# Kernel optimization log

Hardware: AMD Instinct MI355X
Metric: run time of the kernel (lower is better)

Reference implementation:

```python
import jax, jax.numpy as jnp
import numpy as np

NUM_HEADS = 4
KERNEL = 7
DILATION = 1
EMBED = 128
CTX = 256
RANK = 8
HEAD_DIM = EMBED // NUM_HEADS
SCALE = HEAD_DIM ** (-0.5)


def setup_inputs() -> dict:
    key = jax.random.key(0)
    ks = jax.random.split(key, 16)
    B, H, W = 4, 64, 64
    inp = {
        "x": jax.random.normal(ks[0], (B, H, W, EMBED), jnp.float32),
        "context": jax.random.normal(ks[1], (B, CTX), jnp.float32),
        # base QKV linear (torch Linear: y = x @ W.T + b)
        "Wqkv": jax.random.normal(ks[2], (3 * EMBED, EMBED), jnp.float32) * 0.02,
        "bqkv": jax.random.normal(ks[3], (3 * EMBED,), jnp.float32) * 0.02,
        # bilinear LoRA params (init scale 0.01 as in source)
        "A": jax.random.normal(ks[4], (EMBED, RANK), jnp.float32) * 0.01,
        "Blora": jax.random.normal(ks[5], (CTX, RANK), jnp.float32) * 0.01,
        "Vlora": jax.random.normal(ks[6], (3 * EMBED, RANK), jnp.float32) * 0.01,
        # gate MLP: Linear(ctx,16) -> ReLU -> Linear(16,1) -> Sigmoid
        "g1w": jax.random.normal(ks[7], (16, CTX), jnp.float32) * 0.05,
        "g1b": jnp.zeros((16,), jnp.float32),
        "g2w": jnp.full((1, 16), -5.0, jnp.float32) * 0.0 + jax.random.normal(ks[8], (1, 16), jnp.float32) * 0.01 - 5.0 / 16.0,
        "g2b": jnp.full((1,), -5.0, jnp.float32),
        # output projection
        "Wproj": jax.random.normal(ks[9], (EMBED, EMBED), jnp.float32) * 0.02,
        "bproj": jnp.zeros((EMBED,), jnp.float32),
    }
    return inp


def _windows(t, H, W):
    # t: [B, nh, H+2p, W+2p, d] -> [B, nh, H, W, K^2, d]
    ws = []
    for i in range(KERNEL):
        for j in range(KERNEL):
            ws.append(t[:, :, i * DILATION:i * DILATION + H, j * DILATION:j * DILATION + W, :])
    return jnp.stack(ws, axis=4)


def reference(x, context, Wqkv, bqkv, A, Blora, Vlora, g1w, g1b, g2w, g2b, Wproj, bproj):
    B, H, W, C = x.shape
    nh, hd = NUM_HEADS, HEAD_DIM
    # context-modulated QKV: base + alpha * ((xA) * (cB)) V^T
    base = x @ Wqkv.T + bqkv                                   # [B,H,W,3C]
    c_proj = context @ Blora                                   # [B,r]
    delta = ((x @ A) * c_proj[:, None, None, :]) @ Vlora.T     # [B,H,W,3C]
    alpha = jax.nn.sigmoid(jax.nn.relu(context @ g1w.T + g1b) @ g2w.T + g2b)  # [B,1]
    qkv = base + alpha[:, None, None, :] * delta               # [B,H,W,3C]

    qkv = qkv.reshape(B, H, W, 3, nh, hd)
    qkv = jnp.transpose(qkv, (3, 0, 4, 1, 2, 5))               # [3,B,nh,H,W,hd]
    q, k, v = qkv[0], qkv[1], qkv[2]

    pad = DILATION * (KERNEL - 1) // 2
    pw = ((0, 0), (0, 0), (pad, pad), (pad, pad), (0, 0))
    k_p = jnp.pad(k, pw)
    v_p = jnp.pad(v, pw)
    kw = _windows(k_p, H, W)                                   # [B,nh,H,W,K2,hd]
    vw = _windows(v_p, H, W)

    attn = jnp.einsum('bnijd,bnijkd->bnijk', q, kw) * SCALE    # [B,nh,H,W,K2]
    attn = jax.nn.softmax(attn, axis=-1)
    out = jnp.einsum('bnijk,bnijkd->bnijd', attn, vw)          # [B,nh,H,W,hd]

    out = jnp.transpose(out, (0, 2, 3, 1, 4)).reshape(B, H, W, C)
    out = out @ Wproj.T + bproj
    return out
```

## Files before the change

### kernel.cpp

```cpp
#include <hip/hip_runtime.h>
#include <cstddef>

#define CTXDIM 256
#define RANK 8
#define SCALE 0.17677669529663687f
#define WSTRIDE 136

#define WF0 0
#define QS0 8704
#define KL0 17408
#define VT0 53248
#define SMSZ 77824
#define KHEAD 8960
#define VHEAD 8192

typedef _Float16 half8 __attribute__((ext_vector_type(8)));
typedef _Float16 half2_t __attribute__((ext_vector_type(2)));
typedef float floatx4 __attribute__((ext_vector_type(4)));
typedef float floatx16 __attribute__((ext_vector_type(16)));
typedef int intx4 __attribute__((ext_vector_type(4)));

struct Params {
  const float *x, *ctx, *Wqkv, *bqkv, *A, *Blora, *Vlora;
  const float *g1w, *g1b, *g2w, *g2b, *Wproj, *bproj;
  float* out;
};

__device__ __forceinline__ void stage_rows_f16_512(const float* __restrict__ src,
                                                   _Float16* dst, int tid) {
  const int row = tid >> 2;
  const int c0 = (tid & 3) * 32;
  const float* sp = src + (size_t)row * 128 + c0;
  _Float16* dp = dst + row * WSTRIDE + c0;
#pragma unroll
  for (int i = 0; i < 4; ++i) {
    const float4 a = *(const float4*)(sp + i * 8);
    const float4 b = *(const float4*)(sp + i * 8 + 4);
    half8 o;
    o[0] = (_Float16)a.x; o[1] = (_Float16)a.y;
    o[2] = (_Float16)a.z; o[3] = (_Float16)a.w;
    o[4] = (_Float16)b.x; o[5] = (_Float16)b.y;
    o[6] = (_Float16)b.z; o[7] = (_Float16)b.w;
    *(half8*)(dp + i * 8) = o;
  }
}

__device__ __forceinline__ int vta(int d, int k) {
  const int sig = (d + (d >> 3)) & 7;
  return d * 256 + (((k >> 3) ^ sig) << 3) + (k & 7);
}

__device__ __forceinline__ int packh(float x, float y) {
  half2_t h;
  h[0] = (_Float16)x;
  h[1] = (_Float16)y;
  return __builtin_bit_cast(int, h);
}

template <int MT0>
__device__ __forceinline__ floatx16 attn_wave(const _Float16* kls,
                                              const _Float16* vtl,
                                              half8 qb0, half8 qb1,
                                              int m31, int l5, int pi, int pj) {
  const floatx16 zz = {0.f,0.f,0.f,0.f,0.f,0.f,0.f,0.f,
                       0.f,0.f,0.f,0.f,0.f,0.f,0.f,0.f};
  floatx16 acc[5];
#pragma unroll
  for (int mt = 0; mt < 5; ++mt) {
    const int Mt = MT0 + mt;
    const half8 ka0 = *(const half8*)&kls[(Mt * 32 + m31) * 40 + l5 * 8];
    const half8 ka1 = *(const half8*)&kls[(Mt * 32 + m31) * 40 + 16 + l5 * 8];
    floatx16 a = zz;
    a = __builtin_amdgcn_mfma_f32_32x32x16_f16(ka0, qb0, a, 0, 0, 0);
    a = __builtin_amdgcn_mfma_f32_32x32x16_f16(ka1, qb1, a, 0, 0, 0);
    acc[mt] = a;
  }

  bool vR[14];
#pragma unroll
  for (int i = 0; i < 14; ++i) vR[i] = (unsigned)(i - pi) < 7u;
  bool vC[8];
#pragma unroll
  for (int c8 = 0; c8 < 8; ++c8) {
    const int hcv = (c8 & 3) + 8 * (c8 >> 2) + 4 * l5;
    vC[c8] = (unsigned)(hcv - pj) < 7u;
  }

  float mxp[4] = {-1e30f, -1e30f, -1e30f, -1e30f};
#pragma unroll
  for (int mt = 0; mt < 5; ++mt) {
#pragma unroll
    for (int reg = 0; reg < 16; ++reg) {
      const bool v = vR[2 * (MT0 + mt) + (reg >> 3)] &&
                     vC[(reg & 3) + 4 * ((reg >> 2) & 1)];
      const float x = v ? acc[mt][reg] : -1e30f;
      acc[mt][reg] = x;
      mxp[reg & 3] = fmaxf(mxp[reg & 3], x);
    }
  }
  float mx = fmaxf(fmaxf(mxp[0], mxp[1]), fmaxf(mxp[2], mxp[3]));
  mx = fmaxf(mx, __shfl_xor(mx, 32, 64));

  const float SC2 = SCALE * 1.4426950408889634f;
  float sp[4] = {0.f, 0.f, 0.f, 0.f};
#pragma unroll
  for (int mt = 0; mt < 5; ++mt) {
#pragma unroll
    for (int reg = 0; reg < 16; ++reg) {
      const float pv = exp2f((acc[mt][reg] - mx) * SC2);
      acc[mt][reg] = pv;
      sp[reg & 3] += pv;
    }
  }
  float sum = (sp[0] + sp[1]) + (sp[2] + sp[3]);
  sum += __shfl_xor(sum, 32, 64);
  const float inv = 1.f / sum;

  floatx16 oacc = zz;
  const int sigd = (m31 + (m31 >> 3)) & 7;
  const int vbase = m31 * 256;
#pragma unroll
  for (int kk = 0; kk < 10; ++kk) {
    const int ks = MT0 * 2 + kk;
    const int mt = (ks >> 1) - MT0;
    const int r8 = 8 * (ks & 1);
    const int E00 = packh(acc[mt][r8 + 0] * inv, acc[mt][r8 + 1] * inv);
    const int E01 = packh(acc[mt][r8 + 2] * inv, acc[mt][r8 + 3] * inv);
    const int E10 = packh(acc[mt][r8 + 4] * inv, acc[mt][r8 + 5] * inv);
    const int E11 = packh(acc[mt][r8 + 6] * inv, acc[mt][r8 + 7] * inv);
    const int R00 = __shfl_xor(E00, 32, 64);
    const int R01 = __shfl_xor(E01, 32, 64);
    const int R10 = __shfl_xor(E10, 32, 64);
    const int R11 = __shfl_xor(E11, 32, 64);
    const int A0 = l5 ? R10 : E00;
    const int A1 = l5 ? R11 : E01;
    const int A2 = l5 ? E10 : R00;
    const int A3 = l5 ? E11 : R01;
    const intx4 ai = {A0, A1, A2, A3};
    const half8 af = __builtin_bit_cast(half8, ai);
    const half8 vb = *(const half8*)&vtl[vbase + (((2 * ks + l5) ^ sigd) << 3)];
    oacc = __builtin_amdgcn_mfma_f32_32x32x16_f16(af, vb, oacc, 0, 0, 0);
  }
  return oacc;
}

__global__ __launch_bounds__(512, 1) void mono_kernel(Params p) {
  __shared__ __align__(16) _Float16 sm[SMSZ];
  __shared__ float cal_s[8];

  const int bid = blockIdx.x;
  const int tj = bid & 7;
  const int ti = (bid >> 3) & 7;
  const int b  = bid >> 6;
  const int tid = threadIdx.x;
  const int lane = tid & 63;
  const int w = tid >> 6;
  const int m31 = lane & 31;
  const int l5 = lane >> 5;
  const int i0 = ti * 8 - 3;
  const int j0 = tj * 8 - 3;

  _Float16* wfold = sm + WF0;
  _Float16* qs    = sm + QS0;
  _Float16* kls   = sm + KL0;
  _Float16* vtl   = sm + VT0;

  const floatx16 zz = {0.f,0.f,0.f,0.f,0.f,0.f,0.f,0.f,
                       0.f,0.f,0.f,0.f,0.f,0.f,0.f,0.f};
  const int sigd = (m31 + (m31 >> 3)) & 7;

  auto load_xrow = [&](int rowlin, half8* xr) {
#pragma unroll
    for (int ks = 0; ks < 8; ++ks) xr[ks] = (half8){0, 0, 0, 0, 0, 0, 0, 0};
    if (rowlin < 196) {
      const int hr = rowlin / 14;
      const int hc = rowlin - hr * 14;
      const int ii = i0 + hr;
      const int jj = j0 + hc;
      if ((unsigned)ii < 64u && (unsigned)jj < 64u) {
        const float* xp = p.x + (size_t)(b * 4096 + ii * 64 + jj) * 128 + l5 * 8;
#pragma unroll
        for (int ks = 0; ks < 8; ++ks) {
          const float4 a = *(const float4*)(xp + ks * 16);
          const float4 c = *(const float4*)(xp + ks * 16 + 4);
          half8 o;
          o[0] = (_Float16)a.x; o[1] = (_Float16)a.y;
          o[2] = (_Float16)a.z; o[3] = (_Float16)a.w;
          o[4] = (_Float16)c.x; o[5] = (_Float16)c.y;
          o[6] = (_Float16)c.z; o[7] = (_Float16)c.w;
          xr[ks] = o;
        }
      }
    }
  };

  const int mtq = (w & 3) + 1;
  const int chq = w >> 2;
  half8 xrq[8];
  load_xrow(mtq * 32 + m31, xrq);

  if (w == 0) {
    const float c0 = p.ctx[b * CTXDIM + lane];
    const float c1 = p.ctx[b * CTXDIM + 64 + lane];
    const float c2 = p.ctx[b * CTXDIM + 128 + lane];
    const float c3 = p.ctx[b * CTXDIM + 192 + lane];
    float cp[RANK];
#pragma unroll
    for (int r = 0; r < RANK; ++r) {
      float q = c0 * p.Blora[lane * RANK + r] + c1 * p.Blora[(64 + lane) * RANK + r] +
                c2 * p.Blora[(128 + lane) * RANK + r] + c3 * p.Blora[(192 + lane) * RANK + r];
#pragma unroll
      for (int s = 32; s; s >>= 1) q += __shfl_xor(q, s, 64);
      cp[r] = q;
    }
    float gacc = 0.f;
#pragma unroll
    for (int h = 0; h < 16; ++h) {
      float q = c0 * p.g1w[h * CTXDIM + lane] + c1 * p.g1w[h * CTXDIM + 64 + lane] +
                c2 * p.g1w[h * CTXDIM + 128 + lane] + c3 * p.g1w[h * CTXDIM + 192 + lane];
#pragma unroll
      for (int s = 32; s; s >>= 1) q += __shfl_xor(q, s, 64);
      gacc += fmaxf(q + p.g1b[h], 0.f) * p.g2w[h];
    }
    if (lane == 0) {
      const float alpha = 1.f / (1.f + __expf(-(gacc + p.g2b[0])));
#pragma unroll
      for (int r = 0; r < RANK; ++r) cal_s[r] = alpha * cp[r];
    }
  }

  for (int idx = tid; idx < 2688; idx += 512) {
    const int hd = idx / 896;
    const int r2 = idx - hd * 896;
    const int d = r2 & 31;
    const int kk = r2 >> 5;
    const int k = (kk >> 1) * 16 + 14 + (kk & 1);
    vtl[hd * VHEAD + vta(d, k)] = (_Float16)0.f;
  }

  const int kq = tid & 127;
  const int hgrp = tid >> 7;
  const float4 a0 = *(const float4*)&p.A[kq * RANK];
  const float4 a1 = *(const float4*)&p.A[kq * RANK + 4];

  __syncthreads();

  const float* cb = cal_s;
  const float t0 = a0.x * cb[0], t1 = a0.y * cb[1];
  const float t2 = a0.z * cb[2], t3 = a0.w * cb[3];
  const float t4 = a1.x * cb[4], t5 = a1.y * cb[5];
  const float t6 = a1.z * cb[6], t7 = a1.w * cb[7];

  auto FOLD = [&](int n0) {
#pragma unroll
    for (int rr = 0; rr < 16; ++rr) {
      const int row = hgrp * 16 + rr;
      const int o = n0 + row;
      const float4 v0 = *(const float4*)&p.Vlora[o * RANK];
      const float4 v1 = *(const float4*)&p.Vlora[o * RANK + 4];
      float d = t0 * v0.x;
      d = fmaf(t1, v0.y, d);
      d = fmaf(t2, v0.z, d);
      d = fmaf(t3, v0.w, d);
      d = fmaf(t4, v1.x, d);
      d = fmaf(t5, v1.y, d);
      d = fmaf(t6, v1.z, d);
      d = fmaf(t7, v1.w, d);
      wfold[row * WSTRIDE + kq] = (_Float16)(p.Wqkv[o * 128 + kq] + d);
    }
  };

  auto QGEMM = [&](int i) {
    const int n0 = i * 64;
    const int nc = n0 + chq * 32 + m31;
    const float bq = p.bqkv[nc];
    floatx16 c = zz;
    const _Float16* br = &wfold[(chq * 32 + m31) * WSTRIDE + l5 * 8];
#pragma unroll
    for (int ks = 0; ks < 8; ++ks) {
      const half8 f = *(const half8*)(br + ks * 16);
      c = __builtin_amdgcn_mfma_f32_32x32x16_f16(xrq[ks], f, c, 0, 0, 0);
    }
#pragma unroll
    for (int reg = 0; reg < 16; ++reg) {
      const int rowlin = mtq * 32 + (reg & 3) + 8 * (reg >> 2) + 4 * l5;
      const int hr = rowlin / 14;
      const int hc = rowlin - hr * 14;
      if ((unsigned)(hr - 3) < 8u && (unsigned)(hc - 3) < 8u) {
        const int px = (hr - 3) * 8 + (hc - 3);
        qs[px * 136 + nc] = (_Float16)(c[reg] + bq);
      }
    }
  };

  FOLD(0);   __syncthreads(); QGEMM(0); __syncthreads();
  FOLD(64);  __syncthreads(); QGEMM(1); __syncthreads();

  half8 xrkv[8];
  load_xrow(w * 32 + m31, xrkv);
  floatx16 v3save = zz;

  auto KVGEMM = [&](int it) {
    const int n0 = it * 64;
    const float bh0 = p.bqkv[n0 + m31];
    const float bh1 = p.bqkv[n0 + 32 + m31];
    if (w < 7) {
      floatx16 c0 = zz, c1 = zz;
      const _Float16* b0r = &wfold[m31 * WSTRIDE + l5 * 8];
      const _Float16* b1r = &wfold[(32 + m31) * WSTRIDE + l5 * 8];
#pragma unroll
      for (int ks = 0; ks < 8; ++ks) {
        const half8 f0 = *(const half8*)(b0r + ks * 16);
        const half8 f1 = *(const half8*)(b1r + ks * 16);
        c0 = __builtin_amdgcn_mfma_f32_32x32x16_f16(xrkv[ks], f0, c0, 0, 0, 0);
        c1 = __builtin_amdgcn_mfma_f32_32x32x16_f16(xrkv[ks], f1, c1, 0, 0, 0);
      }
#pragma unroll
      for (int reg = 0; reg < 16; ++reg) {
        const int rowlin = w * 32 + (reg & 3) + 8 * (reg >> 2) + 4 * l5;
        if (rowlin < 196) {
          const int hr = rowlin / 14;
          const int hc = rowlin - hr * 14;
          const int hp = hr * 16 + hc;
          const bool ok = (unsigned)(i0 + hr) < 64u && (unsigned)(j0 + hc) < 64u;
          const float v0 = ok ? c0[reg] + bh0 : 0.f;
          const float v1 = ok ? c1[reg] + bh1 : 0.f;
          const int off = (((hp >> 3) ^ sigd) << 3) | (hp & 7);
          if (it == 2) {
            kls[hp * 40 + m31] = (_Float16)v0;
            kls[KHEAD + hp * 40 + m31] = (_Float16)v1;
          } else if (it == 3) {
            kls[2 * KHEAD + hp * 40 + m31] = (_Float16)v0;
            kls[3 * KHEAD + hp * 40 + m31] = (_Float16)v1;
          } else if (it == 4) {
            vtl[m31 * 256 + off] = (_Float16)v0;
            vtl[VHEAD + m31 * 256 + off] = (_Float16)v1;
          } else {
            vtl[2 * VHEAD + m31 * 256 + off] = (_Float16)v0;
            v3save[reg] = v1;
          }
        }
      }
    }
  };

  FOLD(128); __syncthreads(); KVGEMM(2); __syncthreads();
  FOLD(192); __syncthreads(); KVGEMM(3); __syncthreads();
  FOLD(256); __syncthreads(); KVGEMM(4); __syncthreads();
  FOLD(320); __syncthreads(); KVGEMM(5); __syncthreads();

  for (int idx = tid; idx < 896; idx += 512) {
    const int d = idx & 31;
    const int kk = idx >> 5;
    const int k = (kk >> 1) * 16 + 14 + (kk & 1);
    wfold[vta(d, k)] = (_Float16)0.f;
  }
  if (w < 7) {
#pragma unroll
    for (int reg = 0; reg < 16; ++reg) {
      const int rowlin = w * 32 + (reg & 3) + 8 * (reg >> 2) + 4 * l5;
      if (rowlin < 196) {
        const int hr = rowlin / 14;
        const int hc = rowlin - hr * 14;
        const int hp = hr * 16 + hc;
        const int off = (((hp >> 3) ^ sigd) << 3) | (hp & 7);
        wfold[m31 * 256 + off] = (_Float16)v3save[reg];
      }
    }
  }
  __syncthreads();

  const int hh = w >> 1;
  const int half_ = w & 1;
  const int pixA = half_ * 32 + m31;
  const int piA = pixA >> 3, pjA = pixA & 7;
  const half8 qb0 = *(const half8*)&qs[pixA * 136 + hh * 32 + l5 * 8];
  const half8 qb1 = *(const half8*)&qs[pixA * 136 + hh * 32 + 16 + l5 * 8];
  const _Float16* kpp = kls + hh * KHEAD;
  const _Float16* vpp = (hh < 3) ? (vtl + hh * VHEAD) : wfold;

  const floatx16 oA = half_ ? attn_wave<2>(kpp, vpp, qb0, qb1, m31, l5, piA, pjA)
                            : attn_wave<0>(kpp, vpp, qb0, qb1, m31, l5, piA, pjA);
  __syncthreads();

  _Float16* at_s = kls;
  _Float16* wsh  = kls + 64 * WSTRIDE;
#pragma unroll
  for (int reg = 0; reg < 16; ++reg) {
    const int rowM = (reg & 3) + 8 * (reg >> 2) + 4 * l5;
    at_s[(half_ * 32 + rowM) * WSTRIDE + hh * 32 + m31] = (_Float16)oA[reg];
  }
  stage_rows_f16_512(p.Wproj, wsh, tid);
  __syncthreads();

  const int r = lane & 15;
  const int quad = lane >> 4;
  const int rw = w & 3;
  const int nh = w >> 2;
  const _Float16* ap = at_s + (rw * 16 + r) * WSTRIDE + quad * 8;
  const _Float16* bp = wsh + (nh * 64 + r) * WSTRIDE + quad * 8;
  floatx4 acc[4];
#pragma unroll
  for (int nt = 0; nt < 4; ++nt) acc[nt] = (floatx4){0.f, 0.f, 0.f, 0.f};
#pragma unroll
  for (int kc = 0; kc < 4; ++kc) {
    const half8 a = *(const half8*)(ap + kc * 32);
#pragma unroll
    for (int nt = 0; nt < 4; ++nt) {
      const half8 bf = *(const half8*)(bp + nt * 16 * WSTRIDE + kc * 32);
      acc[nt] = __builtin_amdgcn_mfma_f32_16x16x32_f16(a, bf, acc[nt], 0, 0, 0);
    }
  }

  const int rbase = b * 4096 + (ti * 8 + rw * 2 + (quad >> 1)) * 64 +
                    tj * 8 + (quad & 1) * 4;
  float bv[4];
#pragma unroll
  for (int nt = 0; nt < 4; ++nt) bv[nt] = p.bproj[nh * 64 + nt * 16 + r];
#pragma unroll
  for (int reg = 0; reg < 4; ++reg) {
    float* cp = p.out + (size_t)(rbase + reg) * 128 + nh * 64;
#pragma unroll
    for (int nt = 0; nt < 4; ++nt)
      cp[nt * 16 + r] = acc[nt][reg] + bv[nt];
  }
}

extern "C" void kernel_launch(void* const* d_in, const int* in_sizes, int n_in,
                              void* d_out, int out_size, void* d_ws, size_t ws_size,
                              hipStream_t stream) {
  Params hp;
  hp.x     = (const float*)d_in[0];
  hp.ctx   = (const float*)d_in[1];
  hp.Wqkv  = (const float*)d_in[2];
  hp.bqkv  = (const float*)d_in[3];
  hp.A     = (const float*)d_in[4];
  hp.Blora = (const float*)d_in[5];
  hp.Vlora = (const float*)d_in[6];
  hp.g1w   = (const float*)d_in[7];
  hp.g1b   = (const float*)d_in[8];
  hp.g2w   = (const float*)d_in[9];
  hp.g2b   = (const float*)d_in[10];
  hp.Wproj = (const float*)d_in[11];
  hp.bproj = (const float*)d_in[12];
  hp.out   = (float*)d_out;

  mono_kernel<<<256, 512, 0, stream>>>(hp);
}
```

Before: 46.80 us.

## Switch neighborhood attention softmax to online per-tile form with deferred normalization

The per-wave attention now fuses QK scores, masking, exponentiation and the PV MFMA tile by tile, using an online-softmax running max and sum. Rescaling is skipped unless the tile max exceeds the running max by a threshold, and the 1/sum normalization moves to the epilogue store. This removes the five live 32x32 score accumulators, cutting register pressure and the separate max/exp/sum passes. It adds wave-wide votes and shuffles, and launch bounds now request two blocks per CU, which caps registers but may not fit the large LDS footprint.

```diff
diff --git a/kernel.cpp b/kernel.cpp
--- a/kernel.cpp
+++ b/kernel.cpp
@@ -61,10 +61,27 @@
 __device__ __forceinline__ floatx16 attn_wave(const _Float16* kls,
                                               const _Float16* vtl,
                                               half8 qb0, half8 qb1,
-                                              int m31, int l5, int pi, int pj) {
+                                              int m31, int l5, int pi, int pj,
+                                              float& inv_out) {
   const floatx16 zz = {0.f,0.f,0.f,0.f,0.f,0.f,0.f,0.f,
                        0.f,0.f,0.f,0.f,0.f,0.f,0.f,0.f};
-  floatx16 acc[5];
+  bool vR[14];
+#pragma unroll
+  for (int i = 0; i < 14; ++i) vR[i] = (unsigned)(i - pi) < 7u;
+  bool vC[8];
+#pragma unroll
+  for (int c8 = 0; c8 < 8; ++c8) {
+    const int hcv = (c8 & 3) + 8 * (c8 >> 2) + 4 * l5;
+    vC[c8] = (unsigned)(hcv - pj) < 7u;
+  }
+
+  const float SC2 = SCALE * 1.4426950408889634f;
+  const int sigd = (m31 + (m31 >> 3)) & 7;
+  const int vbase = m31 * 256;
+
+  floatx16 oacc = zz;
+  float m = -1e30f, s = 0.f;
+
 #pragma unroll
   for (int mt = 0; mt < 5; ++mt) {
     const int Mt = MT0 + mt;
@@ -73,78 +90,66 @@
     floatx16 a = zz;
     a = __builtin_amdgcn_mfma_f32_32x32x16_f16(ka0, qb0, a, 0, 0, 0);
     a = __builtin_amdgcn_mfma_f32_32x32x16_f16(ka1, qb1, a, 0, 0, 0);
-    acc[mt] = a;
-  }
-
-  bool vR[14];
-#pragma unroll
-  for (int i = 0; i < 14; ++i) vR[i] = (unsigned)(i - pi) < 7u;
-  bool vC[8];
-#pragma unroll
-  for (int c8 = 0; c8 < 8; ++c8) {
-    const int hcv = (c8 & 3) + 8 * (c8 >> 2) + 4 * l5;
-    vC[c8] = (unsigned)(hcv - pj) < 7u;
-  }
-
-  float mxp[4] = {-1e30f, -1e30f, -1e30f, -1e30f};
-#pragma unroll
-  for (int mt = 0; mt < 5; ++mt) {
+
+    float pmax = -1e30f;
 #pragma unroll
     for (int reg = 0; reg < 16; ++reg) {
-      const bool v = vR[2 * (MT0 + mt) + (reg >> 3)] &&
+      const bool v = vR[2 * Mt + (reg >> 3)] &&
                      vC[(reg & 3) + 4 * ((reg >> 2) & 1)];
-      const float x = v ? acc[mt][reg] : -1e30f;
-      acc[mt][reg] = x;
-      mxp[reg & 3] = fmaxf(mxp[reg & 3], x);
-    }
-  }
-  float mx = fmaxf(fmaxf(mxp[0], mxp[1]), fmaxf(mxp[2], mxp[3]));
-  mx = fmaxf(mx, __shfl_xor(mx, 32, 64));
-
-  const float SC2 = SCALE * 1.4426950408889634f;
-  float sp[4] = {0.f, 0.f, 0.f, 0.f};
-#pragma unroll
-  for (int mt = 0; mt < 5; ++mt) {
+      const float x = v ? a[reg] : -1e30f;
+      a[reg] = x;
+      pmax = fmaxf(pmax, x);
+    }
+    const float pmaxp = fmaxf(pmax, __shfl_xor(pmax, 32, 64));
+
+    if (!__all(pmaxp - m <= 16.f)) {
+      const float mnew = fmaxf(m, pmaxp);
+      const float f = exp2f((m - mnew) * SC2);
+      s *= f;
+#pragma unroll
+      for (int reg = 0; reg < 16; ++reg) {
+        const int rowM = (reg & 3) + 8 * (reg >> 2) + 4 * l5;
+        oacc[reg] *= __shfl(f, rowM, 64);
+      }
+      m = mnew;
+    }
+
 #pragma unroll
     for (int reg = 0; reg < 16; ++reg) {
-      const float pv = exp2f((acc[mt][reg] - mx) * SC2);
-      acc[mt][reg] = pv;
-      sp[reg & 3] += pv;
-    }
-  }
-  float sum = (sp[0] + sp[1]) + (sp[2] + sp[3]);
-  sum += __shfl_xor(sum, 32, 64);
-  const float inv = 1.f / sum;
-
-  floatx16 oacc = zz;
-  const int sigd = (m31 + (m31 >> 3)) & 7;
-  const int vbase = m31 * 256;
-#pragma unroll
-  for (int kk = 0; kk < 10; ++kk) {
-    const int ks = MT0 * 2 + kk;
-    const int mt = (ks >> 1) - MT0;
-    const int r8 = 8 * (ks & 1);
-    const int E00 = packh(acc[mt][r8 + 0] * inv, acc[mt][r8 + 1] * inv);
-    const int E01 = packh(acc[mt][r8 + 2] * inv, acc[mt][r8 + 3] * inv);
-    const int E10 = packh(acc[mt][r8 + 4] * inv, acc[mt][r8 + 5] * inv);
-    const int E11 = packh(acc[mt][r8 + 6] * inv, acc[mt][r8 + 7] * inv);
-    const int R00 = __shfl_xor(E00, 32, 64);
-    const int R01 = __shfl_xor(E01, 32, 64);
-    const int R10 = __shfl_xor(E10, 32, 64);
-    const int R11 = __shfl_xor(E11, 32, 64);
-    const int A0 = l5 ? R10 : E00;
-    const int A1 = l5 ? R11 : E01;
-    const int A2 = l5 ? E10 : R00;
-    const int A3 = l5 ? E11 : R01;
-    const intx4 ai = {A0, A1, A2, A3};
-    const half8 af = __builtin_bit_cast(half8, ai);
-    const half8 vb = *(const half8*)&vtl[vbase + (((2 * ks + l5) ^ sigd) << 3)];
-    oacc = __builtin_amdgcn_mfma_f32_32x32x16_f16(af, vb, oacc, 0, 0, 0);
-  }
+      const float pv = (a[reg] > -1e29f) ? exp2f((a[reg] - m) * SC2) : 0.f;
+      a[reg] = pv;
+      s += pv;
+    }
+
+#pragma unroll
+    for (int ks2 = 0; ks2 < 2; ++ks2) {
+      const int ks = 2 * Mt + ks2;
+      const int r8 = 8 * ks2;
+      const int E00 = packh(a[r8 + 0], a[r8 + 1]);
+      const int E01 = packh(a[r8 + 2], a[r8 + 3]);
+      const int E10 = packh(a[r8 + 4], a[r8 + 5]);
+      const int E11 = packh(a[r8 + 6], a[r8 + 7]);
+      const int R00 = __shfl_xor(E00, 32, 64);
+      const int R01 = __shfl_xor(E01, 32, 64);
+      const int R10 = __shfl_xor(E10, 32, 64);
+      const int R11 = __shfl_xor(E11, 32, 64);
+      const int A0 = l5 ? R10 : E00;
+      const int A1 = l5 ? R11 : E01;
+      const int A2 = l5 ? E10 : R00;
+      const int A3 = l5 ? E11 : R01;
+      const intx4 ai = {A0, A1, A2, A3};
+      const half8 af = __builtin_bit_cast(half8, ai);
+      const half8 vb = *(const half8*)&vtl[vbase + (((2 * ks + l5) ^ sigd) << 3)];
+      oacc = __builtin_amdgcn_mfma_f32_32x32x16_f16(af, vb, oacc, 0, 0, 0);
+    }
+  }
+
+  const float st = s + __shfl_xor(s, 32, 64);
+  inv_out = 1.f / st;
   return oacc;
 }
 
-__global__ __launch_bounds__(512, 1) void mono_kernel(Params p) {
+__global__ __launch_bounds__(512, 2) void mono_kernel(Params p) {
   __shared__ __align__(16) _Float16 sm[SMSZ];
   __shared__ float cal_s[8];
 
@@ -379,8 +384,10 @@
   const _Float16* kpp = kls + hh * KHEAD;
   const _Float16* vpp = (hh < 3) ? (vtl + hh * VHEAD) : wfold;
 
-  const floatx16 oA = half_ ? attn_wave<2>(kpp, vpp, qb0, qb1, m31, l5, piA, pjA)
-                            : attn_wave<0>(kpp, vpp, qb0, qb1, m31, l5, piA, pjA);
+  float invA;
+  const floatx16 oA = half_
+      ? attn_wave<2>(kpp, vpp, qb0, qb1, m31, l5, piA, pjA, invA)
+      : attn_wave<0>(kpp, vpp, qb0, qb1, m31, l5, piA, pjA, invA);
   __syncthreads();
 
   _Float16* at_s = kls;
@@ -388,7 +395,8 @@
 #pragma unroll
   for (int reg = 0; reg < 16; ++reg) {
     const int rowM = (reg & 3) + 8 * (reg >> 2) + 4 * l5;
-    at_s[(half_ * 32 + rowM) * WSTRIDE + hh * 32 + m31] = (_Float16)oA[reg];
+    const float invr = __shfl(invA, rowM, 64);
+    at_s[(half_ * 32 + rowM) * WSTRIDE + hh * 32 + m31] = (_Float16)(oA[reg] * invr);
   }
   stage_rows_f16_512(p.Wproj, wsh, tid);
   __syncthreads();
```

Measured after the change: 48.72 us. 4.1% more time.
